# Performance work log

Hardware: AMD Instinct MI355X
Metric: run time of the kernel (lower is better)

The kernel has to match this reference:

```python
import jax, jax.numpy as jnp
import numpy as np
from jax.scipy.special import logsumexp

EPSILON = 0.1
MAX_ITER = 100
LOG_CLAMP = 1e-30  # matches torch _log_safe clamp(min=1e-30)


def setup_inputs() -> dict:
    key = jax.random.key(0)
    k_c, k_a, k_b = jax.random.split(key, 3)
    B, M, N = 16, 2048, 2048
    C = jax.random.uniform(k_c, (B, M, N), dtype=jnp.float32)  # nonnegative cost matrix
    a = jax.random.uniform(k_a, (B, M), dtype=jnp.float32) + 0.1
    a = a / a.sum(axis=1, keepdims=True)  # source marginal, sums to 1 per batch
    b = jax.random.uniform(k_b, (B, N), dtype=jnp.float32) + 0.1
    b = b / b.sum(axis=1, keepdims=True)  # target marginal
    return {"C": C, "a": a, "b": b}


def reference(C, a, b):
    """Log-domain balanced Sinkhorn (SinkhornDistance.forward, epsilon_scaling=False).

    Returns (distance: (B,), P: (B, M, N)).
    Runs a fixed MAX_ITER iterations (the torch early-break with tol=1e-6 is a
    host-sync convergence shortcut to the same fixed point).
    """
    log_a = jnp.log(jnp.clip(a, LOG_CLAMP))  # (B, M)
    log_b = jnp.log(jnp.clip(b, LOG_CLAMP))  # (B, N)
    log_K = -C / EPSILON  # (B, M, N)
    B, M, N = C.shape
    u0 = jnp.zeros((B, M), dtype=C.dtype)
    v0 = jnp.zeros((B, N), dtype=C.dtype)

    def step(carry, _):
        u, v = carry
        u = log_a - logsumexp(log_K + v[:, None, :], axis=2)  # (B, M)
        v = log_b - logsumexp(log_K + u[:, :, None], axis=1)  # (B, N)
        return (u, v), None

    (u, v), _ = jax.lax.scan(step, (u0, v0), None, length=MAX_ITER)
    log_P = u[:, :, None] + log_K + v[:, None, :]  # (B, M, N)
    P = jnp.exp(log_P)
    distance = jnp.sum(P * C, axis=(1, 2))  # (B,)
    return distance, P
```

## Files before the change

### kernel.cpp

```cpp
#include <hip/hip_runtime.h>
#include <hip/hip_fp16.h>

namespace {

constexpr int NB = 16;
constexpr int MM = 2048;
constexpr int NN = 2048;
constexpr float NEG_INV_EPS = -10.0f;
constexpr int ITERS = 100;


struct KHalf {
  const __half* p;
  __device__ __forceinline__ void load8(size_t i, float* o) const {
    uint4 v = *reinterpret_cast<const uint4*>(p + i);
    const __half2* h = reinterpret_cast<const __half2*>(&v);
    float2 f0 = __half22float2(h[0]);
    float2 f1 = __half22float2(h[1]);
    float2 f2 = __half22float2(h[2]);
    float2 f3 = __half22float2(h[3]);
    o[0] = f0.x; o[1] = f0.y; o[2] = f1.x; o[3] = f1.y;
    o[4] = f2.x; o[5] = f2.y; o[6] = f3.x; o[7] = f3.y;
  }
  __device__ __forceinline__ void load4(size_t i, float* o) const {
    uint2 v = *reinterpret_cast<const uint2*>(p + i);
    const __half2* h = reinterpret_cast<const __half2*>(&v);
    float2 f0 = __half22float2(h[0]);
    float2 f1 = __half22float2(h[1]);
    o[0] = f0.x; o[1] = f0.y; o[2] = f1.x; o[3] = f1.y;
  }
};

struct KFromC {
  const float* p;
  __device__ __forceinline__ void load8(size_t i, float* o) const {
    float4 c0 = *reinterpret_cast<const float4*>(p + i);
    float4 c1 = *reinterpret_cast<const float4*>(p + i + 4);
    o[0] = __expf(NEG_INV_EPS * c0.x); o[1] = __expf(NEG_INV_EPS * c0.y);
    o[2] = __expf(NEG_INV_EPS * c0.z); o[3] = __expf(NEG_INV_EPS * c0.w);
    o[4] = __expf(NEG_INV_EPS * c1.x); o[5] = __expf(NEG_INV_EPS * c1.y);
    o[6] = __expf(NEG_INV_EPS * c1.z); o[7] = __expf(NEG_INV_EPS * c1.w);
  }
  __device__ __forceinline__ void load4(size_t i, float* o) const {
    float4 c0 = *reinterpret_cast<const float4*>(p + i);
    o[0] = __expf(NEG_INV_EPS * c0.x); o[1] = __expf(NEG_INV_EPS * c0.y);
    o[2] = __expf(NEG_INV_EPS * c0.z); o[3] = __expf(NEG_INV_EPS * c0.w);
  }
};


__global__ void __launch_bounds__(256) build_k(const float* __restrict__ C,
                                               __half* __restrict__ K) {
  const size_t stride = (size_t)gridDim.x * blockDim.x * 8;
  const size_t total = (size_t)NB * MM * NN;
  for (size_t i = ((size_t)blockIdx.x * blockDim.x + threadIdx.x) * 8;
       i < total; i += stride) {
    float4 c0 = *reinterpret_cast<const float4*>(C + i);
    float4 c1 = *reinterpret_cast<const float4*>(C + i + 4);
    __half2 h[4];
    h[0] = __floats2half2_rn(__expf(NEG_INV_EPS * c0.x), __expf(NEG_INV_EPS * c0.y));
    h[1] = __floats2half2_rn(__expf(NEG_INV_EPS * c0.z), __expf(NEG_INV_EPS * c0.w));
    h[2] = __floats2half2_rn(__expf(NEG_INV_EPS * c1.x), __expf(NEG_INV_EPS * c1.y));
    h[3] = __floats2half2_rn(__expf(NEG_INV_EPS * c1.z), __expf(NEG_INV_EPS * c1.w));
    *reinterpret_cast<uint4*>(K + i) = *reinterpret_cast<uint4*>(h);
  }
}


template <class KS>
__global__ void __launch_bounds__(512, 4) sink_iter(KS ks,
    const float* __restrict__ a, const float* __restrict__ bm,
    const float* __restrict__ s_cur, float* __restrict__ s_acc,
    float* __restrict__ s_zero, float* __restrict__ z_out) {
  __shared__ __align__(16) float wsh[NN];
  __shared__ float zsh[16];
  const int b = blockIdx.x >> 5;
  const int chunk = blockIdx.x & 31;
  const int tid = threadIdx.x;
  const int bbase = b * NN;

  {
    const float4 b4 = *reinterpret_cast<const float4*>(bm + bbase + tid * 4);
    const float4 s4 = *reinterpret_cast<const float4*>(s_cur + bbase + tid * 4);
    float4 w4;
    w4.x = b4.x * __builtin_amdgcn_rcpf(s4.x);
    w4.y = b4.y * __builtin_amdgcn_rcpf(s4.y);
    w4.z = b4.z * __builtin_amdgcn_rcpf(s4.z);
    w4.w = b4.w * __builtin_amdgcn_rcpf(s4.w);
    *reinterpret_cast<float4*>(&wsh[tid * 4]) = w4;
  }
  if (tid < 64) s_zero[bbase + chunk * 64 + tid] = 0.0f;
  __syncthreads();

  const int wave = tid >> 6;
  const int lane = tid & 63;

  float wreg[32];
#pragma unroll
  for (int k = 0; k < 4; ++k) {
    const float4* w4 = reinterpret_cast<const float4*>(&wsh[k * 512 + lane * 8]);
    const float4 wa = w4[0], wb = w4[1];
    wreg[k * 8 + 0] = wa.x; wreg[k * 8 + 1] = wa.y;
    wreg[k * 8 + 2] = wa.z; wreg[k * 8 + 3] = wa.w;
    wreg[k * 8 + 4] = wb.x; wreg[k * 8 + 5] = wb.y;
    wreg[k * 8 + 6] = wb.z; wreg[k * 8 + 7] = wb.w;
  }

  const int r0 = chunk * 64;
  const int mycol = tid * 4;
  float colacc[4] = {0.f, 0.f, 0.f, 0.f};

  for (int sc = 0; sc < 4; ++sc) {
    const int rowbase = r0 + sc * 16;
#pragma unroll
    for (int rr = 0; rr < 2; ++rr) {
      const int row = rowbase + wave * 2 + rr;
      const size_t kb = ((size_t)(b * MM + row)) * NN;
      float acc = 0.f;
#pragma unroll
      for (int k = 0; k < 4; ++k) {
        float kv[8];
        ks.load8(kb + k * 512 + lane * 8, kv);
#pragma unroll
        for (int m = 0; m < 8; ++m) acc += kv[m] * wreg[k * 8 + m];
      }
#pragma unroll
      for (int off = 32; off; off >>= 1) acc += __shfl_xor(acc, off, 64);
      if (lane == 0) {
        const float zv = a[b * MM + row] * __builtin_amdgcn_rcpf(acc);
        zsh[wave * 2 + rr] = zv;
        z_out[b * MM + row] = zv;
      }
    }
    __syncthreads();
#pragma unroll 4
    for (int r = 0; r < 16; ++r) {
      const float zi = zsh[r];
      float kv[4];
      ks.load4(((size_t)(b * MM + rowbase + r)) * NN + mycol, kv);
#pragma unroll
      for (int m = 0; m < 4; ++m) colacc[m] += kv[m] * zi;
    }
    __syncthreads();
  }

  float* s = s_acc + bbase + mycol;
#pragma unroll
  for (int m = 0; m < 4; ++m) atomicAdd(&s[m], colacc[m]);
}


__global__ void __launch_bounds__(256) final_pass(const float* __restrict__ C,
    const float* __restrict__ z, const float* __restrict__ bm,
    const float* __restrict__ s_fin, float* __restrict__ out) {
  __shared__ __align__(16) float wsh[NN];
  __shared__ float zsh[16];
  __shared__ float red[256];
  const int b = blockIdx.x >> 7;
  const int rc = blockIdx.x & 127;
  const int tid = threadIdx.x;
  const int bbase = b * NN;

  for (int j = tid; j < NN; j += 256)
    wsh[j] = bm[bbase + j] * __builtin_amdgcn_rcpf(s_fin[bbase + j]);
  if (tid < 16) zsh[tid] = z[b * MM + rc * 16 + tid];
  __syncthreads();

  float* __restrict__ P = out + NB;
  const int col = tid * 8;
  const float4* w4 = reinterpret_cast<const float4*>(&wsh[col]);
  const float4 wa = w4[0], wb = w4[1];

  float accd = 0.0f;
#pragma unroll 4
  for (int rr = 0; rr < 16; ++rr) {
    const int row = rc * 16 + rr;
    const float zi = zsh[rr];
    const size_t base = ((size_t)(b * MM + row)) * NN + col;
    float4 c0 = *reinterpret_cast<const float4*>(C + base);
    float4 c1 = *reinterpret_cast<const float4*>(C + base + 4);
    float4 p0, p1;
    p0.x = zi * __expf(NEG_INV_EPS * c0.x) * wa.x;
    p0.y = zi * __expf(NEG_INV_EPS * c0.y) * wa.y;
    p0.z = zi * __expf(NEG_INV_EPS * c0.z) * wa.z;
    p0.w = zi * __expf(NEG_INV_EPS * c0.w) * wa.w;
    p1.x = zi * __expf(NEG_INV_EPS * c1.x) * wb.x;
    p1.y = zi * __expf(NEG_INV_EPS * c1.y) * wb.y;
    p1.z = zi * __expf(NEG_INV_EPS * c1.z) * wb.z;
    p1.w = zi * __expf(NEG_INV_EPS * c1.w) * wb.w;
    *reinterpret_cast<float4*>(P + base) = p0;
    *reinterpret_cast<float4*>(P + base + 4) = p1;
    accd += p0.x * c0.x + p0.y * c0.y + p0.z * c0.z + p0.w * c0.w +
            p1.x * c1.x + p1.y * c1.y + p1.z * c1.z + p1.w * c1.w;
  }

  red[tid] = accd;
  __syncthreads();
  if (tid < 128) red[tid] += red[tid + 128];
  __syncthreads();
  if (tid < 64) {
    float v = red[tid] + red[tid + 64];
#pragma unroll
    for (int off = 32; off; off >>= 1) v += __shfl_xor(v, off, 64);
    if (tid == 0) atomicAdd(&out[b], v);
  }
}

}

extern "C" void kernel_launch(void* const* d_in, const int* in_sizes, int n_in,
                              void* d_out, int out_size, void* d_ws, size_t ws_size,
                              hipStream_t stream) {
  const float* C  = (const float*)d_in[0];
  const float* a  = (const float*)d_in[1];
  const float* bm = (const float*)d_in[2];
  float* out = (float*)d_out;
  char* ws = (char*)d_ws;

  const size_t VEC = (size_t)NB * MM * sizeof(float);
  float* z = (float*)(ws);
  float* s[3] = {(float*)(ws + VEC), (float*)(ws + 2 * VEC), (float*)(ws + 3 * VEC)};
  __half* K = (__half*)(ws + 4 * VEC);
  const size_t needK = 4 * VEC + (size_t)NB * MM * NN * sizeof(__half);
  const bool useHalf = (ws_size >= needK);

  hipMemsetAsync(out, 0, NB * sizeof(float), stream);
  hipMemcpyAsync(s[0], bm, (size_t)NB * NN * sizeof(float),
                 hipMemcpyDeviceToDevice, stream);
  hipMemsetAsync(s[1], 0, (size_t)NB * NN * sizeof(float), stream);

  if (useHalf) {
    build_k<<<8192, 256, 0, stream>>>(C, K);
    KHalf ks{K};
    for (int t = 0; t < ITERS; ++t) {
      sink_iter<KHalf><<<NB * 32, 512, 0, stream>>>(
          ks, a, bm, s[t % 3], s[(t + 1) % 3], s[(t + 2) % 3], z);
    }
  } else {
    KFromC ks{C};
    for (int t = 0; t < ITERS; ++t) {
      sink_iter<KFromC><<<NB * 32, 512, 0, stream>>>(
          ks, a, bm, s[t % 3], s[(t + 1) % 3], s[(t + 2) % 3], z);
    }
  }

  final_pass<<<NB * 128, 256, 0, stream>>>(C, z, bm, s[ITERS % 3], out);
}
```

Baseline: 4.424 ms.

## Fuse row and column passes per row, reusing loaded K tile

Each wave now keeps its 8 rows' K values in registers and uses them twice: once for the row dot product that yields z, and once to accumulate column sums scaled by z. This removes the second global read of K for the column pass and the per-16-row block barriers. The per-wave column partials are reduced through shared-memory atomics (with a lane rotation to spread bank conflicts) before the global atomics. In exchange, register use grows a lot (32 column accumulators plus 32 K values), and occupancy is lowered to 2 blocks per CU through the launch bounds.

New measurement: 7.903 ms. 1.79x slower.

```diff
diff --git a/kernel.cpp b/kernel.cpp
--- a/kernel.cpp
+++ b/kernel.cpp
@@ -22,13 +22,6 @@
     o[0] = f0.x; o[1] = f0.y; o[2] = f1.x; o[3] = f1.y;
     o[4] = f2.x; o[5] = f2.y; o[6] = f3.x; o[7] = f3.y;
   }
-  __device__ __forceinline__ void load4(size_t i, float* o) const {
-    uint2 v = *reinterpret_cast<const uint2*>(p + i);
-    const __half2* h = reinterpret_cast<const __half2*>(&v);
-    float2 f0 = __half22float2(h[0]);
-    float2 f1 = __half22float2(h[1]);
-    o[0] = f0.x; o[1] = f0.y; o[2] = f1.x; o[3] = f1.y;
-  }
 };
 
 struct KFromC {
@@ -40,11 +33,6 @@
     o[2] = __expf(NEG_INV_EPS * c0.z); o[3] = __expf(NEG_INV_EPS * c0.w);
     o[4] = __expf(NEG_INV_EPS * c1.x); o[5] = __expf(NEG_INV_EPS * c1.y);
     o[6] = __expf(NEG_INV_EPS * c1.z); o[7] = __expf(NEG_INV_EPS * c1.w);
-  }
-  __device__ __forceinline__ void load4(size_t i, float* o) const {
-    float4 c0 = *reinterpret_cast<const float4*>(p + i);
-    o[0] = __expf(NEG_INV_EPS * c0.x); o[1] = __expf(NEG_INV_EPS * c0.y);
-    o[2] = __expf(NEG_INV_EPS * c0.z); o[3] = __expf(NEG_INV_EPS * c0.w);
   }
 };
 
@@ -68,12 +56,11 @@
 
 
 template <class KS>
-__global__ void __launch_bounds__(512, 4) sink_iter(KS ks,
+__global__ void __launch_bounds__(512, 2) sink_iter(KS ks,
     const float* __restrict__ a, const float* __restrict__ bm,
     const float* __restrict__ s_cur, float* __restrict__ s_acc,
     float* __restrict__ s_zero, float* __restrict__ z_out) {
   __shared__ __align__(16) float wsh[NN];
-  __shared__ float zsh[16];
   const int b = blockIdx.x >> 5;
   const int chunk = blockIdx.x & 31;
   const int tid = threadIdx.x;
@@ -105,48 +92,58 @@
     wreg[k * 8 + 4] = wb.x; wreg[k * 8 + 5] = wb.y;
     wreg[k * 8 + 6] = wb.z; wreg[k * 8 + 7] = wb.w;
   }
-
-  const int r0 = chunk * 64;
-  const int mycol = tid * 4;
-  float colacc[4] = {0.f, 0.f, 0.f, 0.f};
-
-  for (int sc = 0; sc < 4; ++sc) {
-    const int rowbase = r0 + sc * 16;
-#pragma unroll
-    for (int rr = 0; rr < 2; ++rr) {
-      const int row = rowbase + wave * 2 + rr;
-      const size_t kb = ((size_t)(b * MM + row)) * NN;
-      float acc = 0.f;
-#pragma unroll
-      for (int k = 0; k < 4; ++k) {
-        float kv[8];
-        ks.load8(kb + k * 512 + lane * 8, kv);
-#pragma unroll
-        for (int m = 0; m < 8; ++m) acc += kv[m] * wreg[k * 8 + m];
-      }
-#pragma unroll
-      for (int off = 32; off; off >>= 1) acc += __shfl_xor(acc, off, 64);
-      if (lane == 0) {
-        const float zv = a[b * MM + row] * __builtin_amdgcn_rcpf(acc);
-        zsh[wave * 2 + rr] = zv;
-        z_out[b * MM + row] = zv;
-      }
+  __syncthreads();
+
+  *reinterpret_cast<float4*>(&wsh[tid * 4]) = make_float4(0.f, 0.f, 0.f, 0.f);
+
+  const int r0 = chunk * 64 + wave * 8;
+  const size_t abase = (size_t)b * MM;
+  float colacc[32];
+#pragma unroll
+  for (int j = 0; j < 32; ++j) colacc[j] = 0.f;
+
+#pragma unroll 2
+  for (int rr = 0; rr < 8; ++rr) {
+    const int row = r0 + rr;
+    const size_t kb = ((size_t)(b * MM + row)) * NN;
+    float kvf[32];
+#pragma unroll
+    for (int k = 0; k < 4; ++k) ks.load8(kb + k * 512 + lane * 8, &kvf[k * 8]);
+    float acc0 = 0.f, acc1 = 0.f;
+#pragma unroll
+    for (int j = 0; j < 16; ++j) {
+      acc0 += kvf[2 * j] * wreg[2 * j];
+      acc1 += kvf[2 * j + 1] * wreg[2 * j + 1];
     }
-    __syncthreads();
-#pragma unroll 4
-    for (int r = 0; r < 16; ++r) {
-      const float zi = zsh[r];
-      float kv[4];
-      ks.load4(((size_t)(b * MM + rowbase + r)) * NN + mycol, kv);
-#pragma unroll
-      for (int m = 0; m < 4; ++m) colacc[m] += kv[m] * zi;
-    }
-    __syncthreads();
-  }
-
-  float* s = s_acc + bbase + mycol;
-#pragma unroll
-  for (int m = 0; m < 4; ++m) atomicAdd(&s[m], colacc[m]);
+    float acc = acc0 + acc1;
+#pragma unroll
+    for (int off = 32; off; off >>= 1) acc += __shfl_xor(acc, off, 64);
+    const float zv = a[abase + row] * __builtin_amdgcn_rcpf(acc);
+    if (lane == 0) z_out[abase + row] = zv;
+#pragma unroll
+    for (int j = 0; j < 32; ++j) colacc[j] += kvf[j] * zv;
+  }
+
+  __syncthreads();
+
+  const int rot = (lane >> 2) & 7;
+#pragma unroll
+  for (int mm = 0; mm < 8; ++mm) {
+    const int m = (mm + rot) & 7;
+#pragma unroll
+    for (int k = 0; k < 4; ++k)
+      atomicAdd(&wsh[k * 512 + lane * 8 + m], colacc[k * 8 + m]);
+  }
+  __syncthreads();
+
+  {
+    const float4 cs = *reinterpret_cast<const float4*>(&wsh[tid * 4]);
+    float* s = s_acc + bbase + tid * 4;
+    atomicAdd(&s[0], cs.x);
+    atomicAdd(&s[1], cs.y);
+    atomicAdd(&s[2], cs.z);
+    atomicAdd(&s[3], cs.w);
+  }
 }
 
 
```

## Stage K row tiles in shared memory to reuse across row and column passes

Applied to the files above, without the earlier changes.

The row-sum pass now writes each loaded 16-row half-precision K tile into a 64KB shared buffer, and the column pass reads it from there instead of reloading from global memory. This removes the second global/L2 read of K per iteration. It raises shared memory use per block to about 72KB, which can cut occupancy below the 4 blocks per CU the launch bounds request. On the fallback path K is also quantized to fp16 for the column pass.

Result: faster. 3.612 ms (-18.4%).

```diff
diff --git a/kernel.cpp b/kernel.cpp
--- a/kernel.cpp
+++ b/kernel.cpp
@@ -12,8 +12,9 @@
 
 struct KHalf {
   const __half* p;
-  __device__ __forceinline__ void load8(size_t i, float* o) const {
+  __device__ __forceinline__ void load8h(size_t i, float* o, uint4* raw) const {
     uint4 v = *reinterpret_cast<const uint4*>(p + i);
+    *raw = v;
     const __half2* h = reinterpret_cast<const __half2*>(&v);
     float2 f0 = __half22float2(h[0]);
     float2 f1 = __half22float2(h[1]);
@@ -22,29 +23,23 @@
     o[0] = f0.x; o[1] = f0.y; o[2] = f1.x; o[3] = f1.y;
     o[4] = f2.x; o[5] = f2.y; o[6] = f3.x; o[7] = f3.y;
   }
-  __device__ __forceinline__ void load4(size_t i, float* o) const {
-    uint2 v = *reinterpret_cast<const uint2*>(p + i);
-    const __half2* h = reinterpret_cast<const __half2*>(&v);
-    float2 f0 = __half22float2(h[0]);
-    float2 f1 = __half22float2(h[1]);
-    o[0] = f0.x; o[1] = f0.y; o[2] = f1.x; o[3] = f1.y;
-  }
 };
 
 struct KFromC {
   const float* p;
-  __device__ __forceinline__ void load8(size_t i, float* o) const {
+  __device__ __forceinline__ void load8h(size_t i, float* o, uint4* raw) const {
     float4 c0 = *reinterpret_cast<const float4*>(p + i);
     float4 c1 = *reinterpret_cast<const float4*>(p + i + 4);
     o[0] = __expf(NEG_INV_EPS * c0.x); o[1] = __expf(NEG_INV_EPS * c0.y);
     o[2] = __expf(NEG_INV_EPS * c0.z); o[3] = __expf(NEG_INV_EPS * c0.w);
     o[4] = __expf(NEG_INV_EPS * c1.x); o[5] = __expf(NEG_INV_EPS * c1.y);
     o[6] = __expf(NEG_INV_EPS * c1.z); o[7] = __expf(NEG_INV_EPS * c1.w);
-  }
-  __device__ __forceinline__ void load4(size_t i, float* o) const {
-    float4 c0 = *reinterpret_cast<const float4*>(p + i);
-    o[0] = __expf(NEG_INV_EPS * c0.x); o[1] = __expf(NEG_INV_EPS * c0.y);
-    o[2] = __expf(NEG_INV_EPS * c0.z); o[3] = __expf(NEG_INV_EPS * c0.w);
+    __half2 h[4];
+    h[0] = __floats2half2_rn(o[0], o[1]);
+    h[1] = __floats2half2_rn(o[2], o[3]);
+    h[2] = __floats2half2_rn(o[4], o[5]);
+    h[3] = __floats2half2_rn(o[6], o[7]);
+    *raw = *reinterpret_cast<uint4*>(h);
   }
 };
 
@@ -72,6 +67,7 @@
     const float* __restrict__ a, const float* __restrict__ bm,
     const float* __restrict__ s_cur, float* __restrict__ s_acc,
     float* __restrict__ s_zero, float* __restrict__ z_out) {
+  __shared__ __align__(16) __half ksh[16][NN];
   __shared__ __align__(16) float wsh[NN];
   __shared__ float zsh[16];
   const int b = blockIdx.x >> 5;
@@ -114,13 +110,16 @@
     const int rowbase = r0 + sc * 16;
 #pragma unroll
     for (int rr = 0; rr < 2; ++rr) {
-      const int row = rowbase + wave * 2 + rr;
+      const int lrow = wave * 2 + rr;
+      const int row = rowbase + lrow;
       const size_t kb = ((size_t)(b * MM + row)) * NN;
       float acc = 0.f;
 #pragma unroll
       for (int k = 0; k < 4; ++k) {
         float kv[8];
-        ks.load8(kb + k * 512 + lane * 8, kv);
+        uint4 raw;
+        ks.load8h(kb + k * 512 + lane * 8, kv, &raw);
+        *reinterpret_cast<uint4*>(&ksh[lrow][k * 512 + lane * 8]) = raw;
 #pragma unroll
         for (int m = 0; m < 8; ++m) acc += kv[m] * wreg[k * 8 + m];
       }
@@ -128,7 +127,7 @@
       for (int off = 32; off; off >>= 1) acc += __shfl_xor(acc, off, 64);
       if (lane == 0) {
         const float zv = a[b * MM + row] * __builtin_amdgcn_rcpf(acc);
-        zsh[wave * 2 + rr] = zv;
+        zsh[lrow] = zv;
         z_out[b * MM + row] = zv;
       }
     }
@@ -136,10 +135,14 @@
 #pragma unroll 4
     for (int r = 0; r < 16; ++r) {
       const float zi = zsh[r];
-      float kv[4];
-      ks.load4(((size_t)(b * MM + rowbase + r)) * NN + mycol, kv);
-#pragma unroll
-      for (int m = 0; m < 4; ++m) colacc[m] += kv[m] * zi;
+      uint2 rv = *reinterpret_cast<const uint2*>(&ksh[r][mycol]);
+      const __half2* h = reinterpret_cast<const __half2*>(&rv);
+      const float2 f01 = __half22float2(h[0]);
+      const float2 f23 = __half22float2(h[1]);
+      colacc[0] += f01.x * zi;
+      colacc[1] += f01.y * zi;
+      colacc[2] += f23.x * zi;
+      colacc[3] += f23.y * zi;
     }
     __syncthreads();
   }
```
